# Kernel optimization log

Measured on AMD Instinct MI355X. Metric: run time of the kernel, lower is better.

Reference implementation:

```python
import jax, jax.numpy as jnp
import numpy as np

IN_DIM, OUT_DIM, NUM, K = 128, 128, 5, 3
SIZE = IN_DIM * OUT_DIM  # number of spline activations
BATCH = 1024


def extend_grid(grid, k):
    # pykan: pad grid by k uniform steps on each side -> (size, num+1+2k)
    h = (grid[:, -1:] - grid[:, :1]) / (grid.shape[1] - 1)
    for _ in range(k):
        grid = jnp.concatenate([grid[:, :1] - h, grid, grid[:, -1:] + h], axis=1)
    return grid


def b_batch(x, grid, k):
    # Cox-de-Boor recursion, unrolled over fixed order k.
    # x: (size, batch), grid: (size, P) already extended. Returns (size, P-1-k, batch).
    x = x[:, None, :]        # (size, 1, batch)
    g = grid[:, :, None]     # (size, P, 1)
    B = ((x >= g[:, :-1]) & (x < g[:, 1:])).astype(x.dtype)  # order 0
    for p in range(1, k + 1):
        B = (x - g[:, :-(p + 1)]) / (g[:, p:-1] - g[:, :-(p + 1)]) * B[:, :-1] \
          + (g[:, p + 1:] - x) / (g[:, p + 1:] - g[:, 1:-p]) * B[:, 1:]
    return B


def setup_inputs() -> dict:
    key = jax.random.key(0)
    k1, k2 = jax.random.split(key)
    x = jax.random.normal(k1, (BATCH, IN_DIM), dtype=jnp.float32)
    # grid: identical uniform rows, as in torch.einsum('i,j->ij', ones(size), linspace)
    grid = jnp.tile(jnp.linspace(-1.0, 1.0, NUM + 1, dtype=jnp.float32)[None, :], (SIZE, 1))
    # coef: (size, num+k) spline coefficients (stand-in for curve2coef init)
    coef = jax.random.normal(k2, (SIZE, NUM + K), dtype=jnp.float32) * 0.1
    scale_base = jnp.ones((SIZE,), jnp.float32)
    scale_sp = jnp.ones((SIZE,), jnp.float32)
    mask = jnp.ones((SIZE,), jnp.float32)
    return {"x": x, "grid": grid, "coef": coef,
            "scale_base": scale_base, "scale_sp": scale_sp, "mask": mask}


def reference(x, grid, coef, scale_base, scale_sp, mask):
    batch = x.shape[0]
    # fan out x over out_dim: einsum('ij,k->ikj').reshape(batch,size).T -> (size, batch)
    xe = jnp.broadcast_to(x[:, None, :], (batch, OUT_DIM, IN_DIM)).reshape(batch, SIZE).T
    preacts = xe.T.reshape(batch, OUT_DIM, IN_DIM)
    base = jax.nn.silu(xe).T                                   # (batch, size)
    B = b_batch(xe, extend_grid(grid, K), K)                   # (size, num+k, batch)
    spline = jnp.einsum('ij,ijk->ik', coef, B).T               # (batch, size)
    postspline = spline.reshape(batch, OUT_DIM, IN_DIM)
    y = mask[None, :] * (scale_base[None, :] * base + scale_sp[None, :] * spline)
    postacts = y.reshape(batch, OUT_DIM, IN_DIM)
    y_out = postacts.sum(axis=2)                               # (batch, out_dim)
    return y_out, preacts, postacts, postspline
```

## Files before the change

### kernel.cpp

```cpp
#include <hip/hip_runtime.h>


#define IN_DIM  128
#define OUT_DIM 128
#define NUMG    5
#define KORD    3
#define NB      8
#define SIZE    (IN_DIM * OUT_DIM)
#define BATCH   1024
#define G       8
#define JB      8
#define NBG     (BATCH / G)
#define NJO     (OUT_DIM / JB)
#define WSROW   (10 * IN_DIM)
#define RCHUNK  16

__device__ __forceinline__ void basis_row(const float* __restrict__ grid,
                                          int i, float xv, float* __restrict__ B,
                                          float& silu)
{
    float gr[NUMG + 1];
    #pragma unroll
    for (int rr = 0; rr <= NUMG; ++rr) gr[rr] = grid[i * (NUMG + 1) + rr];

    const float h = (gr[NUMG] - gr[0]) * (1.0f / NUMG);
    float t[NUMG + 1 + 2 * KORD];
    t[2] = gr[0] - h; t[1] = t[2] - h; t[0] = t[1] - h;
    #pragma unroll
    for (int rr = 0; rr <= NUMG; ++rr) t[KORD + rr] = gr[rr];
    t[9] = gr[NUMG] + h; t[10] = t[9] + h; t[11] = t[10] + h;

    float rcp1[11], rcp2[10], rcp3[9];
    #pragma unroll
    for (int m = 0; m < 11; ++m) rcp1[m] = 1.0f / (t[m + 1] - t[m]);
    #pragma unroll
    for (int m = 0; m < 10; ++m) rcp2[m] = 1.0f / (t[m + 2] - t[m]);
    #pragma unroll
    for (int m = 0; m < 9;  ++m) rcp3[m] = 1.0f / (t[m + 3] - t[m]);

    float Bt[NUMG + 2 * KORD];
    #pragma unroll
    for (int m = 0; m < NUMG + 2 * KORD; ++m)
        Bt[m] = (xv >= t[m] && xv < t[m + 1]) ? 1.0f : 0.0f;
    #pragma unroll
    for (int m = 0; m < 10; ++m)
        Bt[m] = (xv - t[m]) * rcp1[m] * Bt[m]
              + (t[m + 2] - xv) * rcp1[m + 1] * Bt[m + 1];
    #pragma unroll
    for (int m = 0; m < 9; ++m)
        Bt[m] = (xv - t[m]) * rcp2[m] * Bt[m]
              + (t[m + 3] - xv) * rcp2[m + 1] * Bt[m + 1];
    #pragma unroll
    for (int m = 0; m < 8; ++m)
        Bt[m] = (xv - t[m]) * rcp3[m] * Bt[m]
              + (t[m + 4] - xv) * rcp3[m + 1] * Bt[m + 1];

    #pragma unroll
    for (int m = 0; m < NB; ++m) B[m] = Bt[m];
    silu = xv / (1.0f + __expf(-xv));
}

__global__ __launch_bounds__(256) void kan_basis(
    const float* __restrict__ x,
    const float* __restrict__ grid,
    float* __restrict__ ws)
{
    const int idx = blockIdx.x * 256 + threadIdx.x;
    const int b = idx >> 7;
    const int i = idx & 127;
    const float xv = x[b * IN_DIM + i];

    float B[NB], silu;
    basis_row(grid, i, xv, B, silu);

    float* wp = ws + (size_t)b * WSROW;
    #pragma unroll
    for (int m = 0; m < NB; ++m) wp[m * IN_DIM + i] = B[m];
    wp[8 * IN_DIM + i] = silu;
    wp[9 * IN_DIM + i] = xv;
}

__global__ __launch_bounds__(256) void kan_stream(
    const float* __restrict__ ws,
    const float* __restrict__ coef,
    const float* __restrict__ scale_base,
    const float* __restrict__ scale_sp,
    const float* __restrict__ mask,
    float* __restrict__ out)
{
    const int tid  = threadIdx.x;
    const int lane = tid & 63;
    const int w    = tid >> 6;
    const int il   = lane & 31;
    const int jh   = lane >> 5;
    const int i4   = il << 2;

    const int jo = blockIdx.x & (NJO - 1);
    const int bc = blockIdx.x >> 4;
    const int j  = jo * JB + w * 2 + jh;

    float4 cfq[8];
    {
        const float4* cp = (const float4*)coef;
        #pragma unroll
        for (int q = 0; q < 8; ++q)
            cfq[q] = cp[(size_t)j * 256 + il * 8 + q];
    }
    const int sS = j * IN_DIM + i4;
    const float4 mkv = *(const float4*)&mask[sS];
    const float4 sbv = *(const float4*)&scale_base[sS];
    const float4 ssv = *(const float4*)&scale_sp[sS];

    float cfs[4][NB];
    #pragma unroll
    for (int k = 0; k < 4; ++k) {
        const float4 lo = cfq[2 * k], hi = cfq[2 * k + 1];
        cfs[k][0] = lo.x; cfs[k][1] = lo.y; cfs[k][2] = lo.z; cfs[k][3] = lo.w;
        cfs[k][4] = hi.x; cfs[k][5] = hi.y; cfs[k][6] = hi.z; cfs[k][7] = hi.w;
    }
    const float mkA[4] = {mkv.x, mkv.y, mkv.z, mkv.w};
    const float sbA[4] = {sbv.x, sbv.y, sbv.z, sbv.w};
    const float ssA[4] = {ssv.x, ssv.y, ssv.z, ssv.w};

    float* out_y   = out;
    float* out_pre = out + BATCH * OUT_DIM;
    float* out_act = out_pre + (size_t)BATCH * SIZE;
    float* out_spl = out_act + (size_t)BATCH * SIZE;

    float py[RCHUNK];

    #pragma unroll
    for (int r = 0; r < RCHUNK; ++r) {
        const int b_r = bc * RCHUNK + r;
        const float* wp = ws + (size_t)b_r * WSROW;

        float4 bas[NB];
        #pragma unroll
        for (int m = 0; m < NB; ++m)
            bas[m] = *(const float4*)&wp[m * IN_DIM + i4];
        const float4 slv = *(const float4*)&wp[8 * IN_DIM + i4];
        const float4 pxv = *(const float4*)&wp[9 * IN_DIM + i4];

        float sp0 = cfs[0][0] * bas[0].x;
        float sp1 = cfs[1][0] * bas[0].y;
        float sp2 = cfs[2][0] * bas[0].z;
        float sp3 = cfs[3][0] * bas[0].w;
        #pragma unroll
        for (int m = 1; m < NB; ++m) {
            const float4 b4 = bas[m];
            sp0 = fmaf(cfs[0][m], b4.x, sp0);
            sp1 = fmaf(cfs[1][m], b4.y, sp1);
            sp2 = fmaf(cfs[2][m], b4.z, sp2);
            sp3 = fmaf(cfs[3][m], b4.w, sp3);
        }

        const float spA[4] = {sp0, sp1, sp2, sp3};
        const float slA[4] = {slv.x, slv.y, slv.z, slv.w};
        float y[4];
        #pragma unroll
        for (int k = 0; k < 4; ++k)
            y[k] = mkA[k] * (sbA[k] * slA[k] + ssA[k] * spA[k]);

        const size_t e = (size_t)b_r * SIZE + (size_t)sS;
        *(float4*)&out_pre[e] = pxv;
        *(float4*)&out_act[e] = make_float4(y[0], y[1], y[2], y[3]);
        *(float4*)&out_spl[e] = make_float4(spA[0], spA[1], spA[2], spA[3]);

        py[r] = (y[0] + y[1]) + (y[2] + y[3]);
    }

    #pragma unroll
    for (int off = 16; off > 0; off >>= 1) {
        #pragma unroll
        for (int r = 0; r < RCHUNK; ++r)
            py[r] += __shfl_down(py[r], off, 32);
    }
    if (il == 0) {
        #pragma unroll
        for (int r = 0; r < RCHUNK; ++r)
            out_y[(bc * RCHUNK + r) * OUT_DIM + j] = py[r];
    }
}

__global__ __launch_bounds__(256) void kan_fused(
    const float* __restrict__ x,
    const float* __restrict__ grid,
    const float* __restrict__ coef,
    const float* __restrict__ scale_base,
    const float* __restrict__ scale_sp,
    const float* __restrict__ mask,
    float* __restrict__ out)
{
    __shared__ float sBT[G][NB][IN_DIM];
    __shared__ float sSilu[G][IN_DIM];
    __shared__ float sXv[G][IN_DIM];

    const int tid = threadIdx.x;
    const int bg  = blockIdx.x >> 4;
    const int jo  = blockIdx.x & (NJO - 1);

    const int lane = tid & 63;
    const int w    = tid >> 6;
    const int il   = lane & 31;
    const int jh   = lane >> 5;
    const int i4   = il << 2;
    const int j    = jo * JB + w * 2 + jh;

    float4 cfq[8];
    {
        const float4* cp = (const float4*)coef;
        #pragma unroll
        for (int q = 0; q < 8; ++q)
            cfq[q] = cp[(size_t)j * 256 + il * 8 + q];
    }
    const int sS = j * IN_DIM + i4;
    const float4 mkv = *(const float4*)&mask[sS];
    const float4 sbv = *(const float4*)&scale_base[sS];
    const float4 ssv = *(const float4*)&scale_sp[sS];

    {
        const int i  = tid & 127;
        const int r0 = tid >> 7;
        #pragma unroll
        for (int it = 0; it < 4; ++it) {
            const int r = it * 2 + r0;
            const float xv = x[(bg * G + r) * IN_DIM + i];
            float B[NB], silu;
            basis_row(grid, i, xv, B, silu);
            #pragma unroll
            for (int m = 0; m < NB; ++m) sBT[r][m][i] = B[m];
            sSilu[r][i] = silu;
            sXv[r][i]   = xv;
        }
    }
    __syncthreads();

    float cfs[4][NB];
    #pragma unroll
    for (int k = 0; k < 4; ++k) {
        const float4 lo = cfq[2 * k], hi = cfq[2 * k + 1];
        cfs[k][0] = lo.x; cfs[k][1] = lo.y; cfs[k][2] = lo.z; cfs[k][3] = lo.w;
        cfs[k][4] = hi.x; cfs[k][5] = hi.y; cfs[k][6] = hi.z; cfs[k][7] = hi.w;
    }
    const float mkA[4] = {mkv.x, mkv.y, mkv.z, mkv.w};
    const float sbA[4] = {sbv.x, sbv.y, sbv.z, sbv.w};
    const float ssA[4] = {ssv.x, ssv.y, ssv.z, ssv.w};

    float* out_y   = out;
    float* out_pre = out + BATCH * OUT_DIM;
    float* out_act = out_pre + (size_t)BATCH * SIZE;
    float* out_spl = out_act + (size_t)BATCH * SIZE;

    float py[G];
    #pragma unroll
    for (int r = 0; r < G; ++r) {
        float4 bas[NB];
        #pragma unroll
        for (int m = 0; m < NB; ++m)
            bas[m] = *(const float4*)&sBT[r][m][i4];

        float sp0 = cfs[0][0] * bas[0].x;
        float sp1 = cfs[1][0] * bas[0].y;
        float sp2 = cfs[2][0] * bas[0].z;
        float sp3 = cfs[3][0] * bas[0].w;
        #pragma unroll
        for (int m = 1; m < NB; ++m) {
            const float4 b4 = bas[m];
            sp0 = fmaf(cfs[0][m], b4.x, sp0);
            sp1 = fmaf(cfs[1][m], b4.y, sp1);
            sp2 = fmaf(cfs[2][m], b4.z, sp2);
            sp3 = fmaf(cfs[3][m], b4.w, sp3);
        }

        const float4 slv = *(const float4*)&sSilu[r][i4];
        const float4 pxv = *(const float4*)&sXv[r][i4];
        const float spA[4] = {sp0, sp1, sp2, sp3};
        const float slA[4] = {slv.x, slv.y, slv.z, slv.w};
        float y[4];
        #pragma unroll
        for (int k = 0; k < 4; ++k)
            y[k] = mkA[k] * (sbA[k] * slA[k] + ssA[k] * spA[k]);

        const int b_r = bg * G + r;
        const size_t e = (size_t)b_r * SIZE + (size_t)sS;
        *(float4*)&out_pre[e] = pxv;
        *(float4*)&out_act[e] = make_float4(y[0], y[1], y[2], y[3]);
        *(float4*)&out_spl[e] = make_float4(spA[0], spA[1], spA[2], spA[3]);

        py[r] = (y[0] + y[1]) + (y[2] + y[3]);
    }

    #pragma unroll
    for (int off = 16; off > 0; off >>= 1) {
        #pragma unroll
        for (int r = 0; r < G; ++r)
            py[r] += __shfl_down(py[r], off, 32);
    }
    if (il == 0) {
        #pragma unroll
        for (int r = 0; r < G; ++r)
            out_y[(bg * G + r) * OUT_DIM + j] = py[r];
    }
}

extern "C" void kernel_launch(void* const* d_in, const int* in_sizes, int n_in,
                              void* d_out, int out_size, void* d_ws, size_t ws_size,
                              hipStream_t stream)
{
    const size_t WS_NEED = (size_t)BATCH * WSROW * sizeof(float);
    if (d_ws != nullptr && ws_size >= WS_NEED) {
        hipLaunchKernelGGL(kan_basis, dim3(BATCH * IN_DIM / 256), dim3(256), 0,
                           stream,
                           (const float*)d_in[0], (const float*)d_in[1],
                           (float*)d_ws);
        hipLaunchKernelGGL(kan_stream, dim3((BATCH / RCHUNK) * NJO), dim3(256),
                           0, stream,
                           (const float*)d_ws, (const float*)d_in[2],
                           (const float*)d_in[3], (const float*)d_in[4],
                           (const float*)d_in[5], (float*)d_out);
    } else {
        hipLaunchKernelGGL(kan_fused, dim3(NJO * NBG), dim3(256), 0, stream,
                           (const float*)d_in[0], (const float*)d_in[1],
                           (const float*)d_in[2], (const float*)d_in[3],
                           (const float*)d_in[4], (const float*)d_in[5],
                           (float*)d_out);
    }
}
```

Baseline: 219.0 us.

## Split streaming kernel into separate preacts, spline, and activation kernels

The single streaming kernel that wrote preacts, postacts and postspline is split into three launches. One copies x directly into preacts, one computes and stores the spline output, and one computes the activations and the row sums. The intent is for each kernel to write a single output stream, which may give cleaner write patterns and less register pressure. In exchange the workspace basis values are read twice, the spline dot product is computed twice, and two extra launches are added.

Measured after the change: 242.0 us. 10.5% more time.

```diff
diff --git a/kernel.cpp b/kernel.cpp
--- a/kernel.cpp
+++ b/kernel.cpp
@@ -80,53 +80,104 @@
     wp[9 * IN_DIM + i] = xv;
 }
 
-__global__ __launch_bounds__(256) void kan_stream(
+__global__ __launch_bounds__(256) void kan_pre(
+    const float* __restrict__ x,
+    float* __restrict__ out_pre)
+{
+    const int b = blockIdx.x;
+    const float4* xr = (const float4*)(x + (size_t)b * IN_DIM);
+    float4* op = (float4*)(out_pre + (size_t)b * SIZE);
+    #pragma unroll
+    for (int k = 0; k < 16; ++k) {
+        const int p = k * 256 + threadIdx.x;
+        op[p] = xr[p & 31];
+    }
+}
+
+#define STREAM_PROLOG                                                     \
+    const int tid  = threadIdx.x;                                         \
+    const int lane = tid & 63;                                            \
+    const int w    = tid >> 6;                                            \
+    const int il   = lane & 31;                                           \
+    const int jh   = lane >> 5;                                           \
+    const int i4   = il << 2;                                             \
+    const int jo = blockIdx.x & (NJO - 1);                                \
+    const int bc = blockIdx.x >> 4;                                       \
+    const int j  = jo * JB + w * 2 + jh;                                  \
+    float4 cfq[8];                                                        \
+    {                                                                     \
+        const float4* cp = (const float4*)coef;                           \
+        _Pragma("unroll")                                                 \
+        for (int q = 0; q < 8; ++q)                                       \
+            cfq[q] = cp[(size_t)j * 256 + il * 8 + q];                    \
+    }                                                                     \
+    const int sS = j * IN_DIM + i4;                                       \
+    float cfs[4][NB];                                                     \
+    _Pragma("unroll")                                                     \
+    for (int k = 0; k < 4; ++k) {                                         \
+        const float4 lo = cfq[2 * k], hi = cfq[2 * k + 1];                \
+        cfs[k][0] = lo.x; cfs[k][1] = lo.y;                               \
+        cfs[k][2] = lo.z; cfs[k][3] = lo.w;                               \
+        cfs[k][4] = hi.x; cfs[k][5] = hi.y;                               \
+        cfs[k][6] = hi.z; cfs[k][7] = hi.w;                               \
+    }
+
+#define DOT4(bas, sp0, sp1, sp2, sp3)                                     \
+    float sp0 = cfs[0][0] * bas[0].x;                                     \
+    float sp1 = cfs[1][0] * bas[0].y;                                     \
+    float sp2 = cfs[2][0] * bas[0].z;                                     \
+    float sp3 = cfs[3][0] * bas[0].w;                                     \
+    _Pragma("unroll")                                                     \
+    for (int m = 1; m < NB; ++m) {                                        \
+        const float4 b4 = bas[m];                                         \
+        sp0 = fmaf(cfs[0][m], b4.x, sp0);                                 \
+        sp1 = fmaf(cfs[1][m], b4.y, sp1);                                 \
+        sp2 = fmaf(cfs[2][m], b4.z, sp2);                                 \
+        sp3 = fmaf(cfs[3][m], b4.w, sp3);                                 \
+    }
+
+__global__ __launch_bounds__(256) void kan_spl(
+    const float* __restrict__ ws,
+    const float* __restrict__ coef,
+    float* __restrict__ out_spl)
+{
+    STREAM_PROLOG
+
+    #pragma unroll
+    for (int r = 0; r < RCHUNK; ++r) {
+        const int b_r = bc * RCHUNK + r;
+        const float* wp = ws + (size_t)b_r * WSROW;
+
+        float4 bas[NB];
+        #pragma unroll
+        for (int m = 0; m < NB; ++m)
+            bas[m] = *(const float4*)&wp[m * IN_DIM + i4];
+
+        DOT4(bas, sp0, sp1, sp2, sp3)
+
+        const size_t e = (size_t)b_r * SIZE + (size_t)sS;
+        *(float4*)&out_spl[e] = make_float4(sp0, sp1, sp2, sp3);
+    }
+}
+
+__global__ __launch_bounds__(256) void kan_act(
     const float* __restrict__ ws,
     const float* __restrict__ coef,
     const float* __restrict__ scale_base,
     const float* __restrict__ scale_sp,
     const float* __restrict__ mask,
-    float* __restrict__ out)
-{
-    const int tid  = threadIdx.x;
-    const int lane = tid & 63;
-    const int w    = tid >> 6;
-    const int il   = lane & 31;
-    const int jh   = lane >> 5;
-    const int i4   = il << 2;
-
-    const int jo = blockIdx.x & (NJO - 1);
-    const int bc = blockIdx.x >> 4;
-    const int j  = jo * JB + w * 2 + jh;
-
-    float4 cfq[8];
-    {
-        const float4* cp = (const float4*)coef;
-        #pragma unroll
-        for (int q = 0; q < 8; ++q)
-            cfq[q] = cp[(size_t)j * 256 + il * 8 + q];
-    }
-    const int sS = j * IN_DIM + i4;
+    float* __restrict__ out_y,
+    float* __restrict__ out_act)
+{
+    STREAM_PROLOG
+
     const float4 mkv = *(const float4*)&mask[sS];
     const float4 sbv = *(const float4*)&scale_base[sS];
     const float4 ssv = *(const float4*)&scale_sp[sS];
-
-    float cfs[4][NB];
-    #pragma unroll
-    for (int k = 0; k < 4; ++k) {
-        const float4 lo = cfq[2 * k], hi = cfq[2 * k + 1];
-        cfs[k][0] = lo.x; cfs[k][1] = lo.y; cfs[k][2] = lo.z; cfs[k][3] = lo.w;
-        cfs[k][4] = hi.x; cfs[k][5] = hi.y; cfs[k][6] = hi.z; cfs[k][7] = hi.w;
-    }
     const float mkA[4] = {mkv.x, mkv.y, mkv.z, mkv.w};
     const float sbA[4] = {sbv.x, sbv.y, sbv.z, sbv.w};
     const float ssA[4] = {ssv.x, ssv.y, ssv.z, ssv.w};
 
-    float* out_y   = out;
-    float* out_pre = out + BATCH * OUT_DIM;
-    float* out_act = out_pre + (size_t)BATCH * SIZE;
-    float* out_spl = out_act + (size_t)BATCH * SIZE;
-
     float py[RCHUNK];
 
     #pragma unroll
@@ -139,20 +190,8 @@
         for (int m = 0; m < NB; ++m)
             bas[m] = *(const float4*)&wp[m * IN_DIM + i4];
         const float4 slv = *(const float4*)&wp[8 * IN_DIM + i4];
-        const float4 pxv = *(const float4*)&wp[9 * IN_DIM + i4];
-
-        float sp0 = cfs[0][0] * bas[0].x;
-        float sp1 = cfs[1][0] * bas[0].y;
-        float sp2 = cfs[2][0] * bas[0].z;
-        float sp3 = cfs[3][0] * bas[0].w;
-        #pragma unroll
-        for (int m = 1; m < NB; ++m) {
-            const float4 b4 = bas[m];
-            sp0 = fmaf(cfs[0][m], b4.x, sp0);
-            sp1 = fmaf(cfs[1][m], b4.y, sp1);
-            sp2 = fmaf(cfs[2][m], b4.z, sp2);
-            sp3 = fmaf(cfs[3][m], b4.w, sp3);
-        }
+
+        DOT4(bas, sp0, sp1, sp2, sp3)
 
         const float spA[4] = {sp0, sp1, sp2, sp3};
         const float slA[4] = {slv.x, slv.y, slv.z, slv.w};
@@ -162,9 +201,7 @@
             y[k] = mkA[k] * (sbA[k] * slA[k] + ssA[k] * spA[k]);
 
         const size_t e = (size_t)b_r * SIZE + (size_t)sS;
-        *(float4*)&out_pre[e] = pxv;
         *(float4*)&out_act[e] = make_float4(y[0], y[1], y[2], y[3]);
-        *(float4*)&out_spl[e] = make_float4(spA[0], spA[1], spA[2], spA[3]);
 
         py[r] = (y[0] + y[1]) + (y[2] + y[3]);
     }
@@ -308,16 +345,26 @@
                               hipStream_t stream)
 {
     const size_t WS_NEED = (size_t)BATCH * WSROW * sizeof(float);
+    float* out_y   = (float*)d_out;
+    float* out_pre = out_y + BATCH * OUT_DIM;
+    float* out_act = out_pre + (size_t)BATCH * SIZE;
+    float* out_spl = out_act + (size_t)BATCH * SIZE;
+
     if (d_ws != nullptr && ws_size >= WS_NEED) {
         hipLaunchKernelGGL(kan_basis, dim3(BATCH * IN_DIM / 256), dim3(256), 0,
                            stream,
                            (const float*)d_in[0], (const float*)d_in[1],
                            (float*)d_ws);
-        hipLaunchKernelGGL(kan_stream, dim3((BATCH / RCHUNK) * NJO), dim3(256),
-                           0, stream,
+        hipLaunchKernelGGL(kan_pre, dim3(BATCH), dim3(256), 0, stream,
+                           (const float*)d_in[0], out_pre);
+        hipLaunchKernelGGL(kan_spl, dim3((BATCH / RCHUNK) * NJO), dim3(256), 0,
+                           stream,
+                           (const float*)d_ws, (const float*)d_in[2], out_spl);
+        hipLaunchKernelGGL(kan_act, dim3((BATCH / RCHUNK) * NJO), dim3(256), 0,
+                           stream,
                            (const float*)d_ws, (const float*)d_in[2],
                            (const float*)d_in[3], (const float*)d_in[4],
-                           (const float*)d_in[5], (float*)d_out);
+                           (const float*)d_in[5], out_y, out_act);
     } else {
         hipLaunchKernelGGL(kan_fused, dim3(NJO * NBG), dim3(256), 0, stream,
                            (const float*)d_in[0], (const float*)d_in[1],
```
